# Kernel optimization log

Hardware: AMD Instinct MI355X
Metric: run time of the kernel (lower is better)

Reference implementation:

```python
import jax, jax.numpy as jnp
import numpy as np

B, S, D, H, MLP_D = 2, 2048, 512, 8, 128
DH = D // H  # 64
EPS = 1e-5


def setup_inputs() -> dict:
    key = jax.random.key(0)
    ks = jax.random.split(key, 8)
    return {
        "z": jax.random.normal(ks[0], (B, S, D), dtype=jnp.float32),
        "head_w": jax.random.normal(ks[1], (H, D, 3 * DH), dtype=jnp.float32),
        "w_o": jax.random.normal(ks[2], (H * DH, D), dtype=jnp.float32),
        "ln_w": jnp.ones((D,), dtype=jnp.float32),
        "ln_b": jnp.zeros((D,), dtype=jnp.float32),
        "w1": jax.random.normal(ks[3], (D, MLP_D), dtype=jnp.float32) * (1.0 / np.sqrt(D)),
        "b1": jnp.zeros((MLP_D,), dtype=jnp.float32),
        "w2": jax.random.normal(ks[4], (MLP_D, D), dtype=jnp.float32) * (1.0 / np.sqrt(MLP_D)),
        "b2": jnp.zeros((D,), dtype=jnp.float32),
    }


def _layernorm(x, w, b):
    mu = jnp.mean(x, axis=-1, keepdims=True)
    var = jnp.var(x, axis=-1, keepdims=True)
    return (x - mu) * jax.lax.rsqrt(var + EPS) * w + b


def reference(z, head_w, w_o, ln_w, ln_b, w1, b1, w2, b2):
    # --- MSA block: z = MSA(LN(z)) + z ---
    x = _layernorm(z, ln_w, ln_b)                       # [B,S,D]
    qkv = jnp.einsum("bsd,hde->bhse", x, head_w)        # [B,H,S,3*DH]
    q, k, v = qkv[..., :DH], qkv[..., DH:2 * DH], qkv[..., 2 * DH:]
    scores = jnp.einsum("bhsd,bhtd->bhst", q, k) / jnp.sqrt(jnp.float32(DH))
    p = jax.nn.softmax(scores, axis=-1)                 # [B,H,S,S]
    o = jnp.einsum("bhst,bhtd->bhsd", p, v)             # [B,H,S,DH]
    # concat heads along last dim (head order matches torch.cat), then project
    o = jnp.transpose(o, (0, 2, 1, 3)).reshape(B, S, H * DH)
    z = o @ w_o + z
    # --- MLP block: z = GELU(Linear2(Linear1(LN(z)))) + z (GELU last, per Sequential) ---
    y = _layernorm(z, ln_w, ln_b)
    y = (y @ w1 + b1) @ w2 + b2
    z = jax.nn.gelu(y, approximate=False) + z
    return z
```

## Files before the change

### kernel.cpp

```cpp
#include <hip/hip_runtime.h>
#include <hip/hip_bf16.h>

typedef unsigned short u16;
typedef unsigned int u32;
typedef __attribute__((ext_vector_type(8))) short short8;
typedef __attribute__((ext_vector_type(8))) __bf16 bf16x8;
typedef __attribute__((ext_vector_type(4))) float f32x4;

#define DEV static __device__ __forceinline__

DEV float bf2f(u16 u) { unsigned v = ((unsigned)u) << 16; float f; __builtin_memcpy(&f, &v, 4); return f; }
DEV u16 f2bf(float f) {
  unsigned u; __builtin_memcpy(&u, &f, 4);
  unsigned lsb = (u >> 16) & 1;
  u += 0x7fffu + lsb;
  return (u16)(u >> 16);
}
DEV float exp2fast(float x) { return __builtin_amdgcn_exp2f(x); }
DEV f32x4 mfma16(short8 a, short8 b, f32x4 c) {
  return __builtin_amdgcn_mfma_f32_16x16x32_bf16(
      __builtin_bit_cast(bf16x8, a), __builtin_bit_cast(bf16x8, b), c, 0, 0, 0);
}
DEV short8 ld8(const u16* p) { return *(const short8*)p; }

__global__ void prep_all(const float* __restrict__ hw, const float* __restrict__ wo,
                         const float* __restrict__ w1, const float* __restrict__ w2,
                         u16* __restrict__ wqh, u16* __restrict__ wql,
                         u16* __restrict__ woT, u16* __restrict__ w1T, u16* __restrict__ w2T) {
  int idx = blockIdx.x * 256 + threadIdx.x;
  if (idx < 786432) {
    int e = idx % 192;
    int d = (idx / 192) % 512;
    int h = idx / (192 * 512);
    float v = hw[idx];
    int n = (e < 64) ? (h * 64 + e) : (e < 128) ? (512 + h * 64 + e - 64) : (1024 + h * 64 + e - 128);
    size_t oi = (size_t)n * 512 + d;
    u16 hh = f2bf(v);
    wqh[oi] = hh;
    if (e < 128) wql[oi] = f2bf(v - bf2f(hh));
  } else if (idx < 786432 + 262144) {
    int i = idx - 786432;
    int n = i % 512, k = i / 512;
    woT[(size_t)n * 512 + k] = f2bf(wo[i]);
  } else if (idx < 786432 + 262144 + 65536) {
    int i = idx - (786432 + 262144);
    int n = i % 128, k = i / 128;
    w1T[(size_t)n * 512 + k] = f2bf(w1[i]);
  } else if (idx < 786432 + 262144 + 131072) {
    int i = idx - (786432 + 262144 + 65536);
    int n = i % 512, k = i / 512;
    w2T[(size_t)n * 128 + k] = f2bf(w2[i]);
  }
}

__global__ __launch_bounds__(256) void ln_kernel(const float* __restrict__ in,
                                                 const float* __restrict__ w,
                                                 const float* __restrict__ bb,
                                                 u16* __restrict__ hi, u16* __restrict__ lo) {
  const int wv = threadIdx.x >> 6, lane = threadIdx.x & 63;
  const int row = blockIdx.x * 4 + wv;
  const float4* r = (const float4*)(in + (size_t)row * 512);
  float4 a0 = r[lane * 2], a1 = r[lane * 2 + 1];
  float s = a0.x + a0.y + a0.z + a0.w + a1.x + a1.y + a1.z + a1.w;
  float ss = a0.x * a0.x + a0.y * a0.y + a0.z * a0.z + a0.w * a0.w +
             a1.x * a1.x + a1.y * a1.y + a1.z * a1.z + a1.w * a1.w;
#pragma unroll
  for (int m = 1; m < 64; m <<= 1) { s += __shfl_xor(s, m); ss += __shfl_xor(ss, m); }
  float mu = s * (1.f / 512.f);
  float var = ss * (1.f / 512.f) - mu * mu;
  float rstd = rsqrtf(var + 1e-5f);
  const float4* wp = (const float4*)w + lane * 2;
  const float4* bp = (const float4*)bb + lane * 2;
  float4 w0 = wp[0], w1v = wp[1], b0 = bp[0], b1v = bp[1];
  float xv[8] = {a0.x, a0.y, a0.z, a0.w, a1.x, a1.y, a1.z, a1.w};
  float wv8[8] = {w0.x, w0.y, w0.z, w0.w, w1v.x, w1v.y, w1v.z, w1v.w};
  float bv8[8] = {b0.x, b0.y, b0.z, b0.w, b1v.x, b1v.y, b1v.z, b1v.w};
  short8 oh, ol;
#pragma unroll
  for (int i = 0; i < 8; i++) {
    float v = (xv[i] - mu) * rstd * wv8[i] + bv8[i];
    u16 hh = f2bf(v);
    oh[i] = (short)hh;
    ol[i] = (short)f2bf(v - bf2f(hh));
  }
  *(short8*)(hi + (size_t)row * 512 + lane * 8) = oh;
  *(short8*)(lo + (size_t)row * 512 + lane * 8) = ol;
}

__global__ __launch_bounds__(256) void gemm_qkv(const u16* __restrict__ Ah, const u16* __restrict__ Alo,
                                                const u16* __restrict__ Bh, const u16* __restrict__ Blo,
                                                u16* __restrict__ qkh, u16* __restrict__ qkl,
                                                u16* __restrict__ vT) {
  __shared__ __align__(16) u16 As[128][40], Asl[128][40], Bs[64][40], Bsl[64][40];
  const int tid = threadIdx.x, lane = tid & 63, wv = tid >> 6;
  const int wm = wv >> 1, wn = wv & 1, g = lane >> 4, r16 = lane & 15;
  const int bm = blockIdx.x * 128, bn = blockIdx.y * 64;
  const bool split = blockIdx.y < 16;
  short8 sA[2], sAl[2], sB, sBl;
  auto ldtile = [&](int kt) {
#pragma unroll
    for (int c = 0; c < 2; c++) {
      int ch = c * 256 + tid;
      sA[c] = ld8(Ah + (size_t)(bm + (ch >> 2)) * 512 + kt + (ch & 3) * 8);
      if (split) sAl[c] = ld8(Alo + (size_t)(bm + (ch >> 2)) * 512 + kt + (ch & 3) * 8);
    }
    sB = ld8(Bh + (size_t)(bn + (tid >> 2)) * 512 + kt + (tid & 3) * 8);
    if (split) sBl = ld8(Blo + (size_t)(bn + (tid >> 2)) * 512 + kt + (tid & 3) * 8);
  };
  f32x4 acc[4][2] = {};
  ldtile(0);
  for (int kt = 0; kt < 512; kt += 32) {
    __syncthreads();
#pragma unroll
    for (int c = 0; c < 2; c++) {
      int ch = c * 256 + tid;
      *(short8*)&As[ch >> 2][(ch & 3) * 8] = sA[c];
      if (split) *(short8*)&Asl[ch >> 2][(ch & 3) * 8] = sAl[c];
    }
    *(short8*)&Bs[tid >> 2][(tid & 3) * 8] = sB;
    if (split) *(short8*)&Bsl[tid >> 2][(tid & 3) * 8] = sBl;
    __syncthreads();
    if (kt + 32 < 512) ldtile(kt + 32);
    short8 af[4], bf_[2], afl[4], bfl[2];
#pragma unroll
    for (int mi = 0; mi < 4; mi++) af[mi] = *(const short8*)&As[wm * 64 + mi * 16 + r16][g * 8];
#pragma unroll
    for (int ni = 0; ni < 2; ni++) bf_[ni] = *(const short8*)&Bs[wn * 32 + ni * 16 + r16][g * 8];
    if (split) {
#pragma unroll
      for (int mi = 0; mi < 4; mi++) afl[mi] = *(const short8*)&Asl[wm * 64 + mi * 16 + r16][g * 8];
#pragma unroll
      for (int ni = 0; ni < 2; ni++) bfl[ni] = *(const short8*)&Bsl[wn * 32 + ni * 16 + r16][g * 8];
    }
#pragma unroll
    for (int mi = 0; mi < 4; mi++)
#pragma unroll
      for (int ni = 0; ni < 2; ni++) {
        acc[mi][ni] = mfma16(af[mi], bf_[ni], acc[mi][ni]);
        if (split) {
          acc[mi][ni] = mfma16(af[mi], bfl[ni], acc[mi][ni]);
          acc[mi][ni] = mfma16(afl[mi], bf_[ni], acc[mi][ni]);
        }
      }
  }
#pragma unroll
  for (int mi = 0; mi < 4; mi++)
#pragma unroll
    for (int ni = 0; ni < 2; ni++) {
      int col = bn + wn * 32 + ni * 16 + r16;
      int row0 = bm + wm * 64 + mi * 16 + g * 4;
      if (split) {
#pragma unroll
        for (int j = 0; j < 4; j++) {
          size_t oi = (size_t)(row0 + j) * 1024 + col;
          float v = acc[mi][ni][j];
          u16 hh = f2bf(v);
          qkh[oi] = hh;
          qkl[oi] = f2bf(v - bf2f(hh));
        }
      } else {
        int vcol = col - 1024;
        ushort4 pk;
        pk.x = f2bf(acc[mi][ni][0]);
        pk.y = f2bf(acc[mi][ni][1]);
        pk.z = f2bf(acc[mi][ni][2]);
        pk.w = f2bf(acc[mi][ni][3]);
        *(ushort4*)(vT + (size_t)vcol * 4096 + row0) = pk;
      }
    }
}

template <int MF, int NF, int EPI>
__global__ __launch_bounds__(256) void gemm_g(const u16* __restrict__ A, const u16* __restrict__ BT,
                                              const float* __restrict__ res, const float* __restrict__ bias,
                                              u16* __restrict__ outb, float* __restrict__ outf,
                                              int N, int K) {
  constexpr int BM = 32 * MF, BN = 32 * NF;
  constexpr int CA = (BM * 4 + 255) / 256, CB = (BN * 4 + 255) / 256;
  __shared__ __align__(16) u16 As[BM][40], Bs[BN][40];
  const int tid = threadIdx.x, lane = tid & 63, wv = tid >> 6;
  const int wm = wv >> 1, wn = wv & 1, g = lane >> 4, r16 = lane & 15;
  const int bm = blockIdx.x * BM, bn = blockIdx.y * BN;
  short8 sA[CA], sB[CB];
  auto ldtile = [&](int kt) {
#pragma unroll
    for (int c = 0; c < CA; c++) {
      int ch = c * 256 + tid;
      if (ch < BM * 4) sA[c] = ld8(A + (size_t)(bm + (ch >> 2)) * K + kt + (ch & 3) * 8);
    }
#pragma unroll
    for (int c = 0; c < CB; c++) {
      int ch = c * 256 + tid;
      if (ch < BN * 4) sB[c] = ld8(BT + (size_t)(bn + (ch >> 2)) * K + kt + (ch & 3) * 8);
    }
  };
  f32x4 acc[MF][NF] = {};
  ldtile(0);
  for (int kt = 0; kt < K; kt += 32) {
    __syncthreads();
#pragma unroll
    for (int c = 0; c < CA; c++) {
      int ch = c * 256 + tid;
      if (ch < BM * 4) *(short8*)&As[ch >> 2][(ch & 3) * 8] = sA[c];
    }
#pragma unroll
    for (int c = 0; c < CB; c++) {
      int ch = c * 256 + tid;
      if (ch < BN * 4) *(short8*)&Bs[ch >> 2][(ch & 3) * 8] = sB[c];
    }
    __syncthreads();
    if (kt + 32 < K) ldtile(kt + 32);
    short8 af[MF], bf_[NF];
#pragma unroll
    for (int mi = 0; mi < MF; mi++) af[mi] = *(const short8*)&As[wm * 16 * MF + mi * 16 + r16][g * 8];
#pragma unroll
    for (int ni = 0; ni < NF; ni++) bf_[ni] = *(const short8*)&Bs[wn * 16 * NF + ni * 16 + r16][g * 8];
#pragma unroll
    for (int mi = 0; mi < MF; mi++)
#pragma unroll
      for (int ni = 0; ni < NF; ni++) acc[mi][ni] = mfma16(af[mi], bf_[ni], acc[mi][ni]);
  }
#pragma unroll
  for (int mi = 0; mi < MF; mi++)
#pragma unroll
    for (int ni = 0; ni < NF; ni++) {
      int col = bn + wn * 16 * NF + ni * 16 + r16;
      int row0 = bm + wm * 16 * MF + mi * 16 + g * 4;
#pragma unroll
      for (int j = 0; j < 4; j++) {
        size_t oi = (size_t)(row0 + j) * N + col;
        float v = acc[mi][ni][j];
        if (EPI == 1) {
          outf[oi] = v + res[oi];
        } else if (EPI == 2) {
          outb[oi] = f2bf(v + bias[col]);
        } else {
          float u = v + bias[col];
          float gl = 0.5f * u * (1.0f + erff(u * 0.70710678118f));
          outf[oi] = gl + res[oi];
        }
      }
    }
}

__global__ __launch_bounds__(256) void attn_kernel(const u16* __restrict__ qkh,
                                                   const u16* __restrict__ qkl,
                                                   const u16* __restrict__ vT,
                                                   u16* __restrict__ o) {
  constexpr int SK = 72, SV = 136, SP = 136;
  __shared__ __align__(16) u16 Kh[128 * SK], Kl[128 * SK], Vt[64 * SV];
  __shared__ __align__(16) u16 Pl[4][16 * SP];
  const int tid = threadIdx.x, lane = tid & 63, w = tid >> 6;
  const int g = lane >> 4, r16 = lane & 15;
  const int qb = blockIdx.x * 64;
  const int b = blockIdx.y >> 3, h = blockIdx.y & 7;
  const size_t bbase = (size_t)b * 2048 * 1024;
  const u16* Qh = qkh + bbase + h * 64;
  const u16* Ql = qkl + bbase + h * 64;
  const u16* KgH = qkh + bbase + 512 + h * 64;
  const u16* KgL = qkl + bbase + 512 + h * 64;
  const u16* Vtg = vT + (size_t)h * 64 * 4096 + (size_t)b * 2048;

  const int qrow = qb + w * 16 + r16;
  short8 qh[2], qlo[2];
#pragma unroll
  for (int ks = 0; ks < 2; ks++) {
    qh[ks] = ld8(Qh + (size_t)qrow * 1024 + ks * 32 + g * 8);
    qlo[ks] = ld8(Ql + (size_t)qrow * 1024 + ks * 32 + g * 8);
  }

  f32x4 oacc[4] = {};
  float m_r = -3e38f, l_r = 0.f;

  const int vd0 = tid >> 4, vkv = (tid & 15) * 8;
  short8 kA[4], kB[4], vS[4];
  auto ldkv = [&](int kt) {
#pragma unroll
    for (int c = 0; c < 4; c++) {
      int ch = c * 256 + tid;
      int kr = ch >> 3, kc = (ch & 7) * 8;
      kA[c] = ld8(KgH + (size_t)(kt + kr) * 1024 + kc);
      kB[c] = ld8(KgL + (size_t)(kt + kr) * 1024 + kc);
    }
#pragma unroll
    for (int c = 0; c < 4; c++)
      vS[c] = ld8(Vtg + (size_t)(vd0 + c * 16) * 4096 + kt + vkv);
  };
  ldkv(0);

  for (int kt = 0; kt < 2048; kt += 128) {
    __syncthreads();
#pragma unroll
    for (int c = 0; c < 4; c++) {
      int ch = c * 256 + tid;
      int kr = ch >> 3, kc = (ch & 7) * 8;
      *(short8*)&Kh[kr * SK + kc] = kA[c];
      *(short8*)&Kl[kr * SK + kc] = kB[c];
    }
#pragma unroll
    for (int c = 0; c < 4; c++)
      *(short8*)&Vt[(vd0 + c * 16) * SV + vkv] = vS[c];
    __syncthreads();
    if (kt + 128 < 2048) ldkv(kt + 128);
    __builtin_amdgcn_s_setprio(1);
    f32x4 s[8];
#pragma unroll
    for (int f = 0; f < 8; f++) {
      s[f] = f32x4{0.f, 0.f, 0.f, 0.f};
#pragma unroll
      for (int ks = 0; ks < 2; ks++) {
        short8 bh = *(const short8*)&Kh[(f * 16 + r16) * SK + ks * 32 + g * 8];
        short8 bl = *(const short8*)&Kl[(f * 16 + r16) * SK + ks * 32 + g * 8];
        s[f] = mfma16(bh, qh[ks], s[f]);
        s[f] = mfma16(bl, qh[ks], s[f]);
        s[f] = mfma16(bh, qlo[ks], s[f]);
      }
    }
    __builtin_amdgcn_s_setprio(0);
    constexpr float SCL2 = 0.125f * 1.44269504f;
    float a[8][4];
    float vm = -3e38f;
#pragma unroll
    for (int f = 0; f < 8; f++)
#pragma unroll
      for (int r = 0; r < 4; r++) {
        a[f][r] = s[f][r] * SCL2;
        vm = fmaxf(vm, a[f][r]);
      }
    vm = fmaxf(vm, __shfl_xor(vm, 16));
    vm = fmaxf(vm, __shfl_xor(vm, 32));
    float mn = fmaxf(m_r, vm);
    float scl = exp2fast(m_r - mn);
    m_r = mn;
    float rs = 0.f;
#pragma unroll
    for (int f = 0; f < 8; f++) {
      float e0 = exp2fast(a[f][0] - mn), e1 = exp2fast(a[f][1] - mn);
      float e2 = exp2fast(a[f][2] - mn), e3 = exp2fast(a[f][3] - mn);
      rs += (e0 + e1) + (e2 + e3);
      u32 u0, u1, u2, u3;
      __builtin_memcpy(&u0, &e0, 4);
      __builtin_memcpy(&u1, &e1, 4);
      __builtin_memcpy(&u2, &e2, 4);
      __builtin_memcpy(&u3, &e3, 4);
      uint2 pk;
      pk.x = (u0 >> 16) | (u1 & 0xFFFF0000u);
      pk.y = (u2 >> 16) | (u3 & 0xFFFF0000u);
      *(uint2*)&Pl[w][r16 * SP + f * 16 + g * 4] = pk;
    }
    rs += __shfl_xor(rs, 16);
    rs += __shfl_xor(rs, 32);
    l_r = l_r * scl + rs;
#pragma unroll
    for (int j = 0; j < 4; j++) {
      float sj = __shfl(scl, (g << 4) + (g << 2) + j);
#pragma unroll
      for (int dt = 0; dt < 4; dt++) oacc[dt][j] *= sj;
    }
    __builtin_amdgcn_s_setprio(1);
#pragma unroll
    for (int ks = 0; ks < 4; ks++) {
      short8 pa = *(const short8*)&Pl[w][r16 * SP + ks * 32 + g * 8];
#pragma unroll
      for (int dt = 0; dt < 4; dt++) {
        short8 vb = *(const short8*)&Vt[(dt * 16 + r16) * SV + ks * 32 + g * 8];
        oacc[dt] = mfma16(pa, vb, oacc[dt]);
      }
    }
    __builtin_amdgcn_s_setprio(0);
  }
#pragma unroll
  for (int j = 0; j < 4; j++) {
    float lj = __shfl(l_r, (g << 4) + (g << 2) + j);
    float il = 1.f / lj;
    int row = b * 2048 + qb + w * 16 + g * 4 + j;
#pragma unroll
    for (int dt = 0; dt < 4; dt++) {
      int col = h * 64 + dt * 16 + r16;
      o[(size_t)row * 512 + col] = f2bf(oacc[dt][j] * il);
    }
  }
}

extern "C" void kernel_launch(void* const* d_in, const int* in_sizes, int n_in,
                              void* d_out, int out_size, void* d_ws, size_t ws_size,
                              hipStream_t stream) {
  const float* z = (const float*)d_in[0];
  const float* head_w = (const float*)d_in[1];
  const float* w_o = (const float*)d_in[2];
  const float* ln_w = (const float*)d_in[3];
  const float* ln_b = (const float*)d_in[4];
  const float* w1 = (const float*)d_in[5];
  const float* b1 = (const float*)d_in[6];
  const float* w2 = (const float*)d_in[7];
  const float* b2 = (const float*)d_in[8];
  float* out = (float*)d_out;

  size_t off = 0;
  auto alc = [&](size_t n) {
    void* p = (char*)d_ws + off;
    off += (n + 255) & ~(size_t)255;
    return p;
  };
  u16* x_hi = (u16*)alc((size_t)4096 * 512 * 2);
  u16* x_lo = (u16*)alc((size_t)4096 * 512 * 2);
  u16* wqh = (u16*)alc((size_t)1536 * 512 * 2);
  u16* wql = (u16*)alc((size_t)1536 * 512 * 2);
  u16* woT = (u16*)alc((size_t)512 * 512 * 2);
  u16* w1T = (u16*)alc((size_t)128 * 512 * 2);
  u16* w2T = (u16*)alc((size_t)512 * 128 * 2);
  u16* qkh = (u16*)alc((size_t)4096 * 1024 * 2);
  u16* qkl = (u16*)alc((size_t)4096 * 1024 * 2);
  u16* vT = (u16*)alc((size_t)512 * 4096 * 2);
  u16* ob = (u16*)alc((size_t)4096 * 512 * 2);
  float* z2 = (float*)alc((size_t)4096 * 512 * 4);
  u16* tb = (u16*)alc((size_t)4096 * 128 * 2);

  prep_all<<<4608, 256, 0, stream>>>(head_w, w_o, w1, w2, wqh, wql, woT, w1T, w2T);

  ln_kernel<<<1024, 256, 0, stream>>>(z, ln_w, ln_b, x_hi, x_lo);

  gemm_qkv<<<dim3(32, 24), 256, 0, stream>>>(x_hi, x_lo, wqh, wql, qkh, qkl, vT);

  attn_kernel<<<dim3(32, 16), 256, 0, stream>>>(qkh, qkl, vT, ob);

  gemm_g<2, 2, 1><<<dim3(64, 8), 256, 0, stream>>>(ob, woT, z, nullptr, nullptr, z2, 512, 512);

  ln_kernel<<<1024, 256, 0, stream>>>(z2, ln_w, ln_b, x_hi, x_lo);

  gemm_g<1, 2, 2><<<dim3(128, 2), 256, 0, stream>>>(x_hi, w1T, nullptr, b1, tb, nullptr, 128, 512);

  gemm_g<2, 2, 3><<<dim3(64, 8), 256, 0, stream>>>(tb, w2T, z2, b2, nullptr, out, 512, 128);
}
```

Measured before the change: 126.4 us.

## Fuse weight prep with first layernorm and skip lazy softmax rescales

Merges the weight-conversion kernel and the first layernorm into one launch by giving extra blocks the layernorm rows, removing one kernel launch and its serialization. In attention, it adds a lazy online-softmax rescale: when no row's new max exceeds the running max by more than 8 (in log2 units), the running max is kept and the O/l rescale with its shuffles is skipped. Exponentials may then reach up to 2^8 before normalization, which still fits in fp32 and bf16 range but slightly changes rounding.

```diff
diff --git a/kernel.cpp b/kernel.cpp
--- a/kernel.cpp
+++ b/kernel.cpp
@@ -23,34 +23,69 @@
 }
 DEV short8 ld8(const u16* p) { return *(const short8*)p; }
 
-__global__ void prep_all(const float* __restrict__ hw, const float* __restrict__ wo,
-                         const float* __restrict__ w1, const float* __restrict__ w2,
-                         u16* __restrict__ wqh, u16* __restrict__ wql,
-                         u16* __restrict__ woT, u16* __restrict__ w1T, u16* __restrict__ w2T) {
-  int idx = blockIdx.x * 256 + threadIdx.x;
-  if (idx < 786432) {
-    int e = idx % 192;
-    int d = (idx / 192) % 512;
-    int h = idx / (192 * 512);
-    float v = hw[idx];
-    int n = (e < 64) ? (h * 64 + e) : (e < 128) ? (512 + h * 64 + e - 64) : (1024 + h * 64 + e - 128);
-    size_t oi = (size_t)n * 512 + d;
+__global__ __launch_bounds__(256) void prep_ln(const float* __restrict__ hw, const float* __restrict__ wo,
+                                               const float* __restrict__ w1, const float* __restrict__ w2,
+                                               u16* __restrict__ wqh, u16* __restrict__ wql,
+                                               u16* __restrict__ woT, u16* __restrict__ w1T,
+                                               u16* __restrict__ w2T,
+                                               const float* __restrict__ zin, const float* __restrict__ lw,
+                                               const float* __restrict__ lb,
+                                               u16* __restrict__ hi, u16* __restrict__ lo) {
+  if (blockIdx.x < 4608) {
+    int idx = blockIdx.x * 256 + threadIdx.x;
+    if (idx < 786432) {
+      int e = idx % 192;
+      int d = (idx / 192) % 512;
+      int h = idx / (192 * 512);
+      float v = hw[idx];
+      int n = (e < 64) ? (h * 64 + e) : (e < 128) ? (512 + h * 64 + e - 64) : (1024 + h * 64 + e - 128);
+      size_t oi = (size_t)n * 512 + d;
+      u16 hh = f2bf(v);
+      wqh[oi] = hh;
+      if (e < 128) wql[oi] = f2bf(v - bf2f(hh));
+    } else if (idx < 786432 + 262144) {
+      int i = idx - 786432;
+      int n = i % 512, k = i / 512;
+      woT[(size_t)n * 512 + k] = f2bf(wo[i]);
+    } else if (idx < 786432 + 262144 + 65536) {
+      int i = idx - (786432 + 262144);
+      int n = i % 128, k = i / 128;
+      w1T[(size_t)n * 512 + k] = f2bf(w1[i]);
+    } else if (idx < 786432 + 262144 + 131072) {
+      int i = idx - (786432 + 262144 + 65536);
+      int n = i % 512, k = i / 512;
+      w2T[(size_t)n * 128 + k] = f2bf(w2[i]);
+    }
+    return;
+  }
+  const int wv = threadIdx.x >> 6, lane = threadIdx.x & 63;
+  const int row = (blockIdx.x - 4608) * 4 + wv;
+  const float4* r = (const float4*)(zin + (size_t)row * 512);
+  float4 a0 = r[lane * 2], a1 = r[lane * 2 + 1];
+  float s = a0.x + a0.y + a0.z + a0.w + a1.x + a1.y + a1.z + a1.w;
+  float ss = a0.x * a0.x + a0.y * a0.y + a0.z * a0.z + a0.w * a0.w +
+             a1.x * a1.x + a1.y * a1.y + a1.z * a1.z + a1.w * a1.w;
+#pragma unroll
+  for (int m = 1; m < 64; m <<= 1) { s += __shfl_xor(s, m); ss += __shfl_xor(ss, m); }
+  float mu = s * (1.f / 512.f);
+  float var = ss * (1.f / 512.f) - mu * mu;
+  float rstd = rsqrtf(var + 1e-5f);
+  const float4* wp = (const float4*)lw + lane * 2;
+  const float4* bp = (const float4*)lb + lane * 2;
+  float4 w0 = wp[0], w1v = wp[1], b0 = bp[0], b1v = bp[1];
+  float xv[8] = {a0.x, a0.y, a0.z, a0.w, a1.x, a1.y, a1.z, a1.w};
+  float wv8[8] = {w0.x, w0.y, w0.z, w0.w, w1v.x, w1v.y, w1v.z, w1v.w};
+  float bv8[8] = {b0.x, b0.y, b0.z, b0.w, b1v.x, b1v.y, b1v.z, b1v.w};
+  short8 oh, ol;
+#pragma unroll
+  for (int i = 0; i < 8; i++) {
+    float v = (xv[i] - mu) * rstd * wv8[i] + bv8[i];
     u16 hh = f2bf(v);
-    wqh[oi] = hh;
-    if (e < 128) wql[oi] = f2bf(v - bf2f(hh));
-  } else if (idx < 786432 + 262144) {
-    int i = idx - 786432;
-    int n = i % 512, k = i / 512;
-    woT[(size_t)n * 512 + k] = f2bf(wo[i]);
-  } else if (idx < 786432 + 262144 + 65536) {
-    int i = idx - (786432 + 262144);
-    int n = i % 128, k = i / 128;
-    w1T[(size_t)n * 512 + k] = f2bf(w1[i]);
-  } else if (idx < 786432 + 262144 + 131072) {
-    int i = idx - (786432 + 262144 + 65536);
-    int n = i % 512, k = i / 512;
-    w2T[(size_t)n * 128 + k] = f2bf(w2[i]);
-  }
+    oh[i] = (short)hh;
+    ol[i] = (short)f2bf(v - bf2f(hh));
+  }
+  *(short8*)(hi + (size_t)row * 512 + lane * 8) = oh;
+  *(short8*)(lo + (size_t)row * 512 + lane * 8) = ol;
 }
 
 __global__ __launch_bounds__(256) void ln_kernel(const float* __restrict__ in,
@@ -329,9 +364,22 @@
       }
     vm = fmaxf(vm, __shfl_xor(vm, 16));
     vm = fmaxf(vm, __shfl_xor(vm, 32));
-    float mn = fmaxf(m_r, vm);
-    float scl = exp2fast(m_r - mn);
-    m_r = mn;
+    const bool skip = __all(vm - m_r <= 8.f);
+    float mn;
+    if (skip) {
+      mn = m_r;
+    } else {
+      mn = fmaxf(m_r, vm);
+      float scl = exp2fast(m_r - mn);
+      m_r = mn;
+      l_r *= scl;
+#pragma unroll
+      for (int j = 0; j < 4; j++) {
+        float sj = __shfl(scl, (g << 4) + (g << 2) + j);
+#pragma unroll
+        for (int dt = 0; dt < 4; dt++) oacc[dt][j] *= sj;
+      }
+    }
     float rs = 0.f;
 #pragma unroll
     for (int f = 0; f < 8; f++) {
@@ -350,13 +398,7 @@
     }
     rs += __shfl_xor(rs, 16);
     rs += __shfl_xor(rs, 32);
-    l_r = l_r * scl + rs;
-#pragma unroll
-    for (int j = 0; j < 4; j++) {
-      float sj = __shfl(scl, (g << 4) + (g << 2) + j);
-#pragma unroll
-      for (int dt = 0; dt < 4; dt++) oacc[dt][j] *= sj;
-    }
+    l_r += rs;
     __builtin_amdgcn_s_setprio(1);
 #pragma unroll
     for (int ks = 0; ks < 4; ks++) {
@@ -416,9 +458,8 @@
   float* z2 = (float*)alc((size_t)4096 * 512 * 4);
   u16* tb = (u16*)alc((size_t)4096 * 128 * 2);
 
-  prep_all<<<4608, 256, 0, stream>>>(head_w, w_o, w1, w2, wqh, wql, woT, w1T, w2T);
-
-  ln_kernel<<<1024, 256, 0, stream>>>(z, ln_w, ln_b, x_hi, x_lo);
+  prep_ln<<<5632, 256, 0, stream>>>(head_w, w_o, w1, w2, wqh, wql, woT, w1T, w2T,
+                                    z, ln_w, ln_b, x_hi, x_lo);
 
   gemm_qkv<<<dim3(32, 24), 256, 0, stream>>>(x_hi, x_lo, wqh, wql, qkh, qkl, vT);
 
```

Result: no change. 124.4 us (-1.6%).
